# Kernel tuning notes

Hardware: AMD Instinct MI355X
Metric: run time of the kernel (lower is better)

Reference implementation:

```python
import jax, jax.numpy as jnp
import numpy as np
from jax import lax

B, T, L, H, K, NL, NB = 32, 512, 2048, 512, 3, 2, 256
PAD = (K - 1) // 2
EPS = 1e-5


def _predictor_params(key):
    k1, k2 = jax.random.split(key)
    s = 1.0 / np.sqrt(H * K).astype(np.float32)
    return dict(
        conv_w=jax.random.normal(k1, (NL, H, H, K), jnp.float32) * s,
        conv_b=jnp.zeros((NL, H), jnp.float32),
        ln_g=jnp.ones((NL, H), jnp.float32),
        ln_b=jnp.zeros((NL, H), jnp.float32),
        lin_w=jax.random.normal(k2, (H, 1), jnp.float32) * 0.02,
        lin_b=jnp.zeros((1,), jnp.float32),
    )


def setup_inputs():
    key = jax.random.key(0)
    ks = jax.random.split(key, 8)
    inp = {
        'x': jax.random.normal(ks[0], (B, T, H), jnp.float32),
        'src_mask': jnp.zeros((B, T), bool),
        'duration_target': jax.random.randint(ks[1], (B, T), 0, 8, jnp.int32),
        'pitch_target': jax.random.normal(ks[2], (B, T), jnp.float32),
        'energy_target': jax.random.uniform(ks[3], (B, T), jnp.float32),
        'max_len': L,
    }
    for name, k in zip(('dur', 'pit', 'en'), ks[4:7]):
        for p, v in _predictor_params(k).items():
            inp[name + '_' + p] = v
    inp['pitch_bins'] = jnp.linspace(-3.0, 3.0, NB - 1)
    inp['energy_bins'] = jnp.linspace(0.0, 1.0, NB - 1)
    k1, k2 = jax.random.split(ks[7])
    inp['pitch_emb'] = jax.random.normal(k1, (NB, H), jnp.float32) * 0.02
    inp['energy_emb'] = jax.random.normal(k2, (NB, H), jnp.float32) * 0.02
    return inp


def _layer_norm(h, g, b):
    m = jnp.mean(h, -1, keepdims=True)
    v = jnp.var(h, -1, keepdims=True)
    return (h - m) * lax.rsqrt(v + EPS) * g + b


def _predictor(x, cw, cb, lg, lb, lw, lbias, mask):
    # stack of [Conv1d(k=3,same) -> ReLU -> LayerNorm] x NL, then Linear -> 1
    out = x
    for i in range(NL):
        h = lax.conv_general_dilated(out.transpose(0, 2, 1), cw[i], (1,), [(PAD, PAD)],
                                     dimension_numbers=('NCH', 'OIH', 'NCH'))
        h = h.transpose(0, 2, 1) + cb[i]  # [B, T, H]
        out = _layer_norm(jax.nn.relu(h), lg[i], lb[i])
    out = (out @ lw)[..., 0] + lbias[0]  # [B, T]
    return jnp.where(mask, 0.0, out)


def _length_regulate(x, duration, max_len):
    # vectorized equivalent of the per-token expand+concat+pad loop
    csum = jnp.cumsum(duration, axis=1)                     # [B, T]
    frames = jnp.arange(max_len)                            # [L]
    idx = jax.vmap(lambda c: jnp.searchsorted(c, frames, side='right'))(csum)  # [B, L]
    idx = jnp.clip(idx, 0, x.shape[1] - 1)
    out = jnp.take_along_axis(x, idx[:, :, None], axis=1)   # [B, L, H]
    mel_len = jnp.minimum(csum[:, -1], max_len)             # [B]
    out = out * (frames[None, :] < mel_len[:, None])[..., None]
    return out, mel_len


def reference(x, src_mask, duration_target, pitch_target, energy_target, max_len,
              dur_conv_w, dur_conv_b, dur_ln_g, dur_ln_b, dur_lin_w, dur_lin_b,
              pit_conv_w, pit_conv_b, pit_ln_g, pit_ln_b, pit_lin_w, pit_lin_b,
              en_conv_w, en_conv_b, en_ln_g, en_ln_b, en_lin_w, en_lin_b,
              pitch_bins, energy_bins, pitch_emb, energy_emb):
    log_d = _predictor(x, dur_conv_w, dur_conv_b, dur_ln_g, dur_ln_b, dur_lin_w, dur_lin_b, src_mask)
    pitch_pred = _predictor(x, pit_conv_w, pit_conv_b, pit_ln_g, pit_ln_b, pit_lin_w, pit_lin_b, src_mask)
    energy_pred = _predictor(x, en_conv_w, en_conv_b, en_ln_g, en_ln_b, en_lin_w, en_lin_b, src_mask)
    # torch.bucketize(target, bins) (right=False) == searchsorted side='left'
    p_emb = pitch_emb[jnp.searchsorted(pitch_bins, pitch_target, side='left')]
    e_emb = energy_emb[jnp.searchsorted(energy_bins, energy_target, side='left')]
    x2 = x + p_emb + e_emb
    out, mel_len = _length_regulate(x2, duration_target, max_len)
    return (out, pitch_pred, energy_pred, log_d, mel_len)
```

## Files before the change

kernel.cpp:

```cpp
#include <hip/hip_runtime.h>
#include <hip/hip_bf16.h>

#define B_ 32
#define T_ 512
#define TP_ 514
#define L_ 2048
#define H_ 512
#define NRR (B_*T_)
#define KC_ 1536
#define NB_ 256
#define EPS_ 1e-5f
#define XPE ((size_t)B_ * TP_ * H_)

typedef __bf16 bf16;
typedef __bf16 bf16x8 __attribute__((ext_vector_type(8)));
typedef float f32x4 __attribute__((ext_vector_type(4)));

static const size_t WC_BYTES  = (size_t)6 * H_ * KC_ * 2;
static const size_t XP_BYTES  = XPE * 2;
static const size_t Y_BYTES   = (size_t)3 * NRR * H_ * 2;

__device__ __forceinline__ void gload16(const void* g, void* l) {
    __builtin_amdgcn_global_load_lds(
        (const __attribute__((address_space(1))) unsigned int*)g,
        (__attribute__((address_space(3))) unsigned int*)l, 16, 0, 0);
}

__global__ void k_prep_wc(const float* __restrict__ wd, const float* __restrict__ wp,
                          const float* __restrict__ we, bf16* __restrict__ wc) {
    int e = blockIdx.x * 256 + threadIdx.x;
    if (e >= 6 * H_ * KC_) return;
    int m   = e / (H_ * KC_);
    int rem = e % (H_ * KC_);
    int o  = rem / KC_;
    int r2 = rem % KC_;
    int k  = r2 / H_;
    int c  = r2 % H_;
    int p = m >> 1, i = m & 1;
    const float* w = (p == 0) ? wd : (p == 1 ? wp : we);
    float v = w[((size_t)i * H_ * H_ + (size_t)o * H_ + c) * 3 + k];
    wc[e] = (bf16)v;
}

__global__ void k_pad(const float* __restrict__ x, bf16* __restrict__ xp0,
                      bf16* __restrict__ xp1) {
    int wid = threadIdx.x >> 6, lane = threadIdx.x & 63;
    int row = blockIdx.x * 4 + wid;
    int b = row / TP_, tp = row % TP_;
    bf16* d0 = xp0 + (size_t)row * H_ + lane * 8;
    if (tp == 0 || tp == TP_ - 1) {
        bf16x8 z;
#pragma unroll
        for (int i = 0; i < 8; ++i) z[i] = (bf16)0.0f;
        *(bf16x8*)d0 = z;
#pragma unroll
        for (int p = 0; p < 3; ++p)
            *(bf16x8*)(xp1 + p * XPE + (size_t)row * H_ + lane * 8) = z;
    } else {
        const f32x4* p = (const f32x4*)(x + ((size_t)(b * T_ + tp - 1)) * H_ + lane * 8);
        f32x4 u = p[0], v = p[1];
        bf16x8 o;
        o[0] = (bf16)u[0]; o[1] = (bf16)u[1]; o[2] = (bf16)u[2]; o[3] = (bf16)u[3];
        o[4] = (bf16)v[0]; o[5] = (bf16)v[1]; o[6] = (bf16)v[2]; o[7] = (bf16)v[3];
        *(bf16x8*)d0 = o;
    }
}

__global__ void k_scan(const int* __restrict__ dur, int* __restrict__ csum,
                       float* __restrict__ mel_out) {
    int b = blockIdx.x, t = threadIdx.x;
    __shared__ int s[T_];
    s[t] = dur[b * T_ + t];
    __syncthreads();
    for (int off = 1; off < T_; off <<= 1) {
        int v = (t >= off) ? s[t - off] : 0;
        __syncthreads();
        s[t] += v;
        __syncthreads();
    }
    csum[b * T_ + t] = s[t];
    if (t == T_ - 1) mel_out[b] = (float)((s[t] < L_) ? s[t] : L_);
}

__global__ void k_gather(const float* __restrict__ x, const float* __restrict__ pemb,
                         const float* __restrict__ eemb, const float* __restrict__ pt,
                         const float* __restrict__ et, const float* __restrict__ pbins,
                         const float* __restrict__ ebins, const int* __restrict__ csum,
                         float* __restrict__ out) {
    int bi = blockIdx.x;
    int b  = bi >> 9;
    int l0 = (bi & 511) << 2;
    __shared__ int cs[T_];
    __shared__ float pb[NB_ - 1], eb[NB_ - 1];
    cs[threadIdx.x]       = csum[b * T_ + threadIdx.x];
    cs[threadIdx.x + 256] = csum[b * T_ + threadIdx.x + 256];
    if (threadIdx.x < NB_ - 1) {
        pb[threadIdx.x] = pbins[threadIdx.x];
        eb[threadIdx.x] = ebins[threadIdx.x];
    }
    __syncthreads();
    int wid = threadIdx.x >> 6, lane = threadIdx.x & 63;
    int l = l0 + wid;
    int mel = cs[T_ - 1]; if (mel > L_) mel = L_;
    float* op = out + ((size_t)(b * L_ + l)) * H_ + lane * 8;
    if (l >= mel) {
        f32x4 z = {0.f, 0.f, 0.f, 0.f};
        ((f32x4*)op)[0] = z;
        ((f32x4*)op)[1] = z;
        return;
    }
    int lo = 0, hi = T_;
    while (lo < hi) { int mid = (lo + hi) >> 1; if (cs[mid] <= l) lo = mid + 1; else hi = mid; }
    int idx = (lo < T_ - 1) ? lo : (T_ - 1);
    int rr = b * T_ + idx;
    float pv = pt[rr], ev = et[rr];
    int pi, ei;
    { int a = 0, c = NB_ - 1; while (a < c) { int mid = (a + c) >> 1; if (pb[mid] < pv) a = mid + 1; else c = mid; } pi = a; }
    { int a = 0, c = NB_ - 1; while (a < c) { int mid = (a + c) >> 1; if (eb[mid] < ev) a = mid + 1; else c = mid; } ei = a; }
    const f32x4* xp = (const f32x4*)(x    + (size_t)rr * H_ + lane * 8);
    const f32x4* pp = (const f32x4*)(pemb + (size_t)pi * H_ + lane * 8);
    const f32x4* ep = (const f32x4*)(eemb + (size_t)ei * H_ + lane * 8);
    ((f32x4*)op)[0] = xp[0] + pp[0] + ep[0];
    ((f32x4*)op)[1] = xp[1] + pp[1] + ep[1];
}

template<int LAYER>
__global__ __launch_bounds__(256)
void k_gemm(const bf16* __restrict__ Xp, const bf16* __restrict__ Wall,
            const float* __restrict__ cb0, const float* __restrict__ cb1,
            const float* __restrict__ cb2, bf16* __restrict__ Y) {
    __shared__ bf16 lA[136 * 64];
    __shared__ bf16 lB[3 * 128 * 64];

    int bid = blockIdx.x;
    int xcd = bid & 7, idx = bid >> 3;
    int colblk = idx >> 4;
    int rowblk = xcd * 16 + (idx & 15);
    int p  = colblk >> 2;
    int oB = (colblk & 3) * 128;
    int rowBase = rowblk * 128;

    const bf16* A = (LAYER == 0) ? Xp : (Xp + (size_t)p * XPE);
    const bf16* W = Wall + ((size_t)(2 * p + LAYER) * H_ + oB) * KC_;
    const float* cbp  = (p == 0) ? cb0 : (p == 1 ? cb1 : cb2);
    const float* bias = cbp + LAYER * H_;

    int tid = threadIdx.x;
    int wid = tid >> 6, lane = tid & 63;
    int wm = wid >> 1, wn = wid & 1;
    int lr = lane & 15, kq = lane >> 4;
    int rsub = lane >> 3;
    int csw  = ((lane & 7) ^ rsub) << 3;
    int b = rowBase >> 9, t0 = rowBase & (T_ - 1);
    const bf16* Abase = A + ((size_t)(b * TP_ + t0)) * H_;

    f32x4 acc[4][4];
#pragma unroll
    for (int m = 0; m < 4; ++m)
#pragma unroll
        for (int n = 0; n < 4; ++n) acc[m][n] = (f32x4){0.f, 0.f, 0.f, 0.f};

    for (int s = 0; s < 8; ++s) {
        int c0 = s * 64;
#pragma unroll
        for (int q = 0; q < 5; ++q) {
            int g = q * 4 + wid;
            if (g < 17)
                gload16(Abase + (size_t)(g * 8 + rsub) * H_ + c0 + csw, &lA[g * 8 * 64]);
        }
#pragma unroll
        for (int tap = 0; tap < 3; ++tap)
#pragma unroll
            for (int q = 0; q < 4; ++q) {
                int g = q * 4 + wid;
                gload16(W + (size_t)(g * 8 + rsub) * KC_ + tap * H_ + c0 + csw,
                        &lB[(tap * 128 + g * 8) * 64]);
            }
        __syncthreads();

#pragma unroll
        for (int tap = 0; tap < 3; ++tap) {
            bf16x8 af[4][2], bfr[4][2];
            int ka = (lr + tap) & 7, kb = lr & 7;
#pragma unroll
            for (int m = 0; m < 4; ++m)
#pragma unroll
                for (int kk = 0; kk < 2; ++kk)
                    af[m][kk] = *(const bf16x8*)&lA[(wm * 64 + m * 16 + lr + tap) * 64 +
                                                    ((((kk * 4 + kq) ^ ka)) << 3)];
#pragma unroll
            for (int n = 0; n < 4; ++n)
#pragma unroll
                for (int kk = 0; kk < 2; ++kk)
                    bfr[n][kk] = *(const bf16x8*)&lB[(tap * 128 + wn * 64 + n * 16 + lr) * 64 +
                                                     ((((kk * 4 + kq) ^ kb)) << 3)];
#pragma unroll
            for (int m = 0; m < 4; ++m)
#pragma unroll
                for (int n = 0; n < 4; ++n)
#pragma unroll
                    for (int kk = 0; kk < 2; ++kk)
                        acc[m][n] = __builtin_amdgcn_mfma_f32_16x16x32_bf16(
                            af[m][kk], bfr[n][kk], acc[m][n], 0, 0, 0);
        }
        __syncthreads();
    }

#pragma unroll
    for (int n = 0; n < 4; ++n) {
        int o = oB + wn * 64 + n * 16 + lr;
        float bi = bias[o];
#pragma unroll
        for (int m = 0; m < 4; ++m) {
            int row = rowBase + wm * 64 + m * 16 + 4 * kq;
#pragma unroll
            for (int r = 0; r < 4; ++r)
                Y[((size_t)p * NRR + row + r) * H_ + o] = (bf16)fmaxf(acc[m][n][r] + bi, 0.f);
        }
    }
}

__global__ void k_ln_store(const bf16* __restrict__ Yin,
                           const float* __restrict__ g0, const float* __restrict__ g1,
                           const float* __restrict__ g2,
                           const float* __restrict__ bb0, const float* __restrict__ bb1,
                           const float* __restrict__ bb2, bf16* __restrict__ xp1) {
    int wid = threadIdx.x >> 6, lane = threadIdx.x & 63;
    int rg = blockIdx.x * 4 + wid;
    int p = rg >> 14, r = rg & (NRR - 1);
    const float* g   = (p == 0) ? g0 : (p == 1 ? g1 : g2);
    const float* bta = (p == 0) ? bb0 : (p == 1 ? bb1 : bb2);
    bf16x8 a = *(const bf16x8*)(Yin + ((size_t)p * NRR + r) * H_ + lane * 8);
    float f[8];
#pragma unroll
    for (int i = 0; i < 8; ++i) f[i] = (float)a[i];
    float s1 = 0.f, s2 = 0.f;
#pragma unroll
    for (int i = 0; i < 8; ++i) { s1 += f[i]; s2 += f[i] * f[i]; }
    for (int m = 1; m < 64; m <<= 1) { s1 += __shfl_xor(s1, m); s2 += __shfl_xor(s2, m); }
    float mean = s1 * (1.f / H_);
    float var  = s2 * (1.f / H_) - mean * mean;
    float rs   = rsqrtf(var + EPS_);
    const f32x4* gp = (const f32x4*)g;
    const f32x4* bp = (const f32x4*)bta;
    f32x4 ga = gp[lane * 2], gb = gp[lane * 2 + 1];
    f32x4 ba = bp[lane * 2], bbv = bp[lane * 2 + 1];
    bf16x8 o;
    o[0] = (bf16)((f[0] - mean) * rs * ga[0] + ba[0]);
    o[1] = (bf16)((f[1] - mean) * rs * ga[1] + ba[1]);
    o[2] = (bf16)((f[2] - mean) * rs * ga[2] + ba[2]);
    o[3] = (bf16)((f[3] - mean) * rs * ga[3] + ba[3]);
    o[4] = (bf16)((f[4] - mean) * rs * gb[0] + bbv[0]);
    o[5] = (bf16)((f[5] - mean) * rs * gb[1] + bbv[1]);
    o[6] = (bf16)((f[6] - mean) * rs * gb[2] + bbv[2]);
    o[7] = (bf16)((f[7] - mean) * rs * gb[3] + bbv[3]);
    int bb = r >> 9, t = r & (T_ - 1);
    *(bf16x8*)(xp1 + (size_t)p * XPE + ((size_t)(bb * TP_ + t + 1)) * H_ + lane * 8) = o;
}

__global__ void k_ln_linear(const bf16* __restrict__ Yin,
                            const float* __restrict__ g0, const float* __restrict__ g1,
                            const float* __restrict__ g2,
                            const float* __restrict__ bb0, const float* __restrict__ bb1,
                            const float* __restrict__ bb2,
                            const float* __restrict__ w0p, const float* __restrict__ w1p,
                            const float* __restrict__ w2p,
                            const float* __restrict__ lb0, const float* __restrict__ lb1,
                            const float* __restrict__ lb2,
                            const unsigned char* __restrict__ mask,
                            float* __restrict__ o0, float* __restrict__ o1,
                            float* __restrict__ o2) {
    int wid = threadIdx.x >> 6, lane = threadIdx.x & 63;
    int rg = blockIdx.x * 4 + wid;
    int p = rg >> 14, r = rg & (NRR - 1);
    const float* g   = ((p == 0) ? g0 : (p == 1 ? g1 : g2)) + H_;
    const float* bta = ((p == 0) ? bb0 : (p == 1 ? bb1 : bb2)) + H_;
    const float* lw  = (p == 0) ? w0p : (p == 1 ? w1p : w2p);
    const float* lb  = (p == 0) ? lb0 : (p == 1 ? lb1 : lb2);
    float*       op  = (p == 0) ? o0 : (p == 1 ? o1 : o2);
    bf16x8 a = *(const bf16x8*)(Yin + ((size_t)p * NRR + r) * H_ + lane * 8);
    float f[8];
#pragma unroll
    for (int i = 0; i < 8; ++i) f[i] = (float)a[i];
    float s1 = 0.f, s2 = 0.f;
#pragma unroll
    for (int i = 0; i < 8; ++i) { s1 += f[i]; s2 += f[i] * f[i]; }
    for (int m = 1; m < 64; m <<= 1) { s1 += __shfl_xor(s1, m); s2 += __shfl_xor(s2, m); }
    float mean = s1 * (1.f / H_);
    float var  = s2 * (1.f / H_) - mean * mean;
    float rs   = rsqrtf(var + EPS_);
    const f32x4* gp = (const f32x4*)g;
    const f32x4* bp = (const f32x4*)bta;
    const f32x4* wp = (const f32x4*)lw;
    f32x4 ga = gp[lane * 2], gb = gp[lane * 2 + 1];
    f32x4 ba = bp[lane * 2], bbv = bp[lane * 2 + 1];
    f32x4 wa = wp[lane * 2], wb = wp[lane * 2 + 1];
    float s = ((f[0] - mean) * rs * ga[0] + ba[0]) * wa[0]
            + ((f[1] - mean) * rs * ga[1] + ba[1]) * wa[1]
            + ((f[2] - mean) * rs * ga[2] + ba[2]) * wa[2]
            + ((f[3] - mean) * rs * ga[3] + ba[3]) * wa[3]
            + ((f[4] - mean) * rs * gb[0] + bbv[0]) * wb[0]
            + ((f[5] - mean) * rs * gb[1] + bbv[1]) * wb[1]
            + ((f[6] - mean) * rs * gb[2] + bbv[2]) * wb[2]
            + ((f[7] - mean) * rs * gb[3] + bbv[3]) * wb[3];
    for (int m = 1; m < 64; m <<= 1) s += __shfl_xor(s, m);
    if (lane == 0) op[r] = mask[r] ? 0.f : (s + lb[0]);
}

extern "C" void kernel_launch(void* const* d_in, const int* in_sizes, int n_in,
                              void* d_out, int out_size, void* d_ws, size_t ws_size,
                              hipStream_t stream) {
    const float* x  = (const float*)d_in[0];
    const unsigned char* mask = (const unsigned char*)d_in[1];
    const int*   dur = (const int*)d_in[2];
    const float* pt  = (const float*)d_in[3];
    const float* et  = (const float*)d_in[4];
    const float* cw[3]    = {(const float*)d_in[6],  (const float*)d_in[12], (const float*)d_in[18]};
    const float* cb[3]    = {(const float*)d_in[7],  (const float*)d_in[13], (const float*)d_in[19]};
    const float* lg[3]    = {(const float*)d_in[8],  (const float*)d_in[14], (const float*)d_in[20]};
    const float* lbn[3]   = {(const float*)d_in[9],  (const float*)d_in[15], (const float*)d_in[21]};
    const float* lw[3]    = {(const float*)d_in[10], (const float*)d_in[16], (const float*)d_in[22]};
    const float* lbias[3] = {(const float*)d_in[11], (const float*)d_in[17], (const float*)d_in[23]};
    const float* pbins = (const float*)d_in[24];
    const float* ebins = (const float*)d_in[25];
    const float* pemb  = (const float*)d_in[26];
    const float* eemb  = (const float*)d_in[27];

    float* out0 = (float*)d_out;
    const size_t OUT0 = (size_t)B_ * L_ * H_;
    float* pitch_out  = out0 + OUT0;
    float* energy_out = pitch_out + NRR;
    float* logd_out   = energy_out + NRR;
    float* mel_out    = logd_out + NRR;

    char* ws = (char*)d_ws;
    bf16*  wc   = (bf16*)ws;
    bf16*  xp0  = (bf16*)(ws + WC_BYTES);
    bf16*  xp1  = (bf16*)(ws + WC_BYTES + XP_BYTES);
    bf16*  y    = (bf16*)(ws + WC_BYTES + 4 * XP_BYTES);
    int*   csum = (int*)(ws + WC_BYTES + 4 * XP_BYTES + Y_BYTES);

    k_prep_wc<<<(6 * H_ * KC_ + 255) / 256, 256, 0, stream>>>(cw[0], cw[1], cw[2], wc);
    k_pad<<<B_ * TP_ / 4, 256, 0, stream>>>(x, xp0, xp1);
    k_scan<<<B_, T_, 0, stream>>>(dur, csum, mel_out);
    k_gather<<<B_ * L_ / 4, 256, 0, stream>>>(x, pemb, eemb, pt, et, pbins, ebins, csum, out0);

    k_gemm<0><<<1536, 256, 0, stream>>>(xp0, wc, cb[0], cb[1], cb[2], y);
    k_ln_store<<<3 * NRR / 4, 256, 0, stream>>>(y, lg[0], lg[1], lg[2],
                                                lbn[0], lbn[1], lbn[2], xp1);
    k_gemm<1><<<1536, 256, 0, stream>>>(xp1, wc, cb[0], cb[1], cb[2], y);
    k_ln_linear<<<3 * NRR / 4, 256, 0, stream>>>(y, lg[0], lg[1], lg[2],
                                                 lbn[0], lbn[1], lbn[2],
                                                 lw[0], lw[1], lw[2],
                                                 lbias[0], lbias[1], lbias[2],
                                                 mask, logd_out, pitch_out, energy_out);
}
```

Baseline: 246.1 us.

## Prepack conv weights in MFMA fragment order and load B directly from global

Weights are repacked during prep into per-column-block sections laid out in the exact per-lane MFMA B-fragment order. The GEMM drops its LDS staging buffer for B and has each lane read its bf16x8 fragments straight from global memory. This cuts LDS traffic and footprint, which could allow more resident blocks. The cost is that every wave now issues its own global/L2 loads for B with no sharing through LDS, and those loads sit on the MFMA critical path.

```diff
diff --git a/kernel.cpp b/kernel.cpp
--- a/kernel.cpp
+++ b/kernel.cpp
@@ -11,6 +11,7 @@
 #define NB_ 256
 #define EPS_ 1e-5f
 #define XPE ((size_t)B_ * TP_ * H_)
+#define WSEC 196608
 
 typedef __bf16 bf16;
 typedef __bf16 bf16x8 __attribute__((ext_vector_type(8)));
@@ -30,16 +31,20 @@
                           const float* __restrict__ we, bf16* __restrict__ wc) {
     int e = blockIdx.x * 256 + threadIdx.x;
     if (e >= 6 * H_ * KC_) return;
-    int m   = e / (H_ * KC_);
-    int rem = e % (H_ * KC_);
-    int o  = rem / KC_;
-    int r2 = rem % KC_;
-    int k  = r2 / H_;
-    int c  = r2 % H_;
+    int sec = e / WSEC, r = e % WSEC;
+    int m = sec >> 2, colblk = sec & 3;
+    int j  = r & 7;
+    int l  = (r >> 3) & 63;
+    int n  = (r >> 9) & 3;
+    int wn = (r >> 11) & 1;
+    int kk = (r >> 12) & 1;
+    int t13 = r >> 13;
+    int tap = t13 % 3, hc = t13 / 3;
+    int o = colblk * 128 + wn * 64 + n * 16 + (l & 15);
+    int c = hc * 64 + kk * 32 + (l >> 4) * 8 + j;
     int p = m >> 1, i = m & 1;
     const float* w = (p == 0) ? wd : (p == 1 ? wp : we);
-    float v = w[((size_t)i * H_ * H_ + (size_t)o * H_ + c) * 3 + k];
-    wc[e] = (bf16)v;
+    wc[e] = (bf16)w[((size_t)(i * H_ + o) * H_ + c) * 3 + tap];
 }
 
 __global__ void k_pad(const float* __restrict__ x, bf16* __restrict__ xp0,
@@ -130,7 +135,6 @@
             const float* __restrict__ cb0, const float* __restrict__ cb1,
             const float* __restrict__ cb2, bf16* __restrict__ Y) {
     __shared__ bf16 lA[136 * 64];
-    __shared__ bf16 lB[3 * 128 * 64];
 
     int bid = blockIdx.x;
     int xcd = bid & 7, idx = bid >> 3;
@@ -141,7 +145,7 @@
     int rowBase = rowblk * 128;
 
     const bf16* A = (LAYER == 0) ? Xp : (Xp + (size_t)p * XPE);
-    const bf16* W = Wall + ((size_t)(2 * p + LAYER) * H_ + oB) * KC_;
+    const bf16* Wsec = Wall + (size_t)((2 * p + LAYER) * 4 + (colblk & 3)) * WSEC;
     const float* cbp  = (p == 0) ? cb0 : (p == 1 ? cb1 : cb2);
     const float* bias = cbp + LAYER * H_;
 
@@ -153,6 +157,7 @@
     int csw  = ((lane & 7) ^ rsub) << 3;
     int b = rowBase >> 9, t0 = rowBase & (T_ - 1);
     const bf16* Abase = A + ((size_t)(b * TP_ + t0)) * H_;
+    const bf16* Wlane = Wsec + (size_t)wn * 2048 + lane * 8;
 
     f32x4 acc[4][4];
 #pragma unroll
@@ -168,32 +173,25 @@
             if (g < 17)
                 gload16(Abase + (size_t)(g * 8 + rsub) * H_ + c0 + csw, &lA[g * 8 * 64]);
         }
-#pragma unroll
-        for (int tap = 0; tap < 3; ++tap)
-#pragma unroll
-            for (int q = 0; q < 4; ++q) {
-                int g = q * 4 + wid;
-                gload16(W + (size_t)(g * 8 + rsub) * KC_ + tap * H_ + c0 + csw,
-                        &lB[(tap * 128 + g * 8) * 64]);
-            }
+        const bf16* Wh = Wlane + (size_t)s * 24576;
         __syncthreads();
 
 #pragma unroll
         for (int tap = 0; tap < 3; ++tap) {
             bf16x8 af[4][2], bfr[4][2];
-            int ka = (lr + tap) & 7, kb = lr & 7;
+            int ka = (lr + tap) & 7;
+#pragma unroll
+            for (int n = 0; n < 4; ++n)
+#pragma unroll
+                for (int kk = 0; kk < 2; ++kk)
+                    bfr[n][kk] = *(const bf16x8*)&Wh[((size_t)(tap * 2 + kk) * 2) * 2048 +
+                                                     n * 512];
 #pragma unroll
             for (int m = 0; m < 4; ++m)
 #pragma unroll
                 for (int kk = 0; kk < 2; ++kk)
                     af[m][kk] = *(const bf16x8*)&lA[(wm * 64 + m * 16 + lr + tap) * 64 +
                                                     ((((kk * 4 + kq) ^ ka)) << 3)];
-#pragma unroll
-            for (int n = 0; n < 4; ++n)
-#pragma unroll
-                for (int kk = 0; kk < 2; ++kk)
-                    bfr[n][kk] = *(const bf16x8*)&lB[(tap * 128 + wn * 64 + n * 16 + lr) * 64 +
-                                                     ((((kk * 4 + kq) ^ kb)) << 3)];
 #pragma unroll
             for (int m = 0; m < 4; ++m)
 #pragma unroll
```

After: 265.2 us. 1.08x slower.

## Fuse layer-2 LayerNorm+Linear reduction into GEMM epilogue via per-row partial sums

Applied to the files above, without the earlier changes.

The second conv GEMM no longer writes its bf16 activations. Its epilogue instead computes per-row partial sums (sum, sum of squares, and a gamma*w-weighted sum) over each 128-column tile and stores them to a small buffer. A tiny finalize kernel then combines the four column-tile partials and applies the LayerNorm+Linear algebraically, folding gamma*w and beta*w into constants. This removes the layer-2 Y write and reread and one full-size kernel, at the cost of extra shuffles and a shared-memory reduction in the epilogue, and variance computed as E[x^2]-mean^2 in fp32.

```diff
diff --git a/kernel.cpp b/kernel.cpp
--- a/kernel.cpp
+++ b/kernel.cpp
@@ -128,7 +128,12 @@
 __global__ __launch_bounds__(256)
 void k_gemm(const bf16* __restrict__ Xp, const bf16* __restrict__ Wall,
             const float* __restrict__ cb0, const float* __restrict__ cb1,
-            const float* __restrict__ cb2, bf16* __restrict__ Y) {
+            const float* __restrict__ cb2,
+            const float* __restrict__ g0, const float* __restrict__ g1,
+            const float* __restrict__ g2,
+            const float* __restrict__ w0p, const float* __restrict__ w1p,
+            const float* __restrict__ w2p,
+            bf16* __restrict__ Y, float* __restrict__ part) {
     __shared__ bf16 lA[136 * 64];
     __shared__ bf16 lB[3 * 128 * 64];
 
@@ -206,16 +211,59 @@
         __syncthreads();
     }
 
-#pragma unroll
-    for (int n = 0; n < 4; ++n) {
-        int o = oB + wn * 64 + n * 16 + lr;
-        float bi = bias[o];
-#pragma unroll
-        for (int m = 0; m < 4; ++m) {
-            int row = rowBase + wm * 64 + m * 16 + 4 * kq;
-#pragma unroll
-            for (int r = 0; r < 4; ++r)
-                Y[((size_t)p * NRR + row + r) * H_ + o] = (bf16)fmaxf(acc[m][n][r] + bi, 0.f);
+    if constexpr (LAYER == 0) {
+#pragma unroll
+        for (int n = 0; n < 4; ++n) {
+            int o = oB + wn * 64 + n * 16 + lr;
+            float bi = bias[o];
+#pragma unroll
+            for (int m = 0; m < 4; ++m) {
+                int row = rowBase + wm * 64 + m * 16 + 4 * kq;
+#pragma unroll
+                for (int r = 0; r < 4; ++r)
+                    Y[((size_t)p * NRR + row + r) * H_ + o] = (bf16)fmaxf(acc[m][n][r] + bi, 0.f);
+            }
+        }
+    } else {
+        const float* gp  = ((p == 0) ? g0 : (p == 1 ? g1 : g2)) + H_;
+        const float* lwp = (p == 0) ? w0p : (p == 1 ? w1p : w2p);
+        float bc[4], gc[4], wc4[4];
+#pragma unroll
+        for (int n = 0; n < 4; ++n) {
+            int col = oB + wn * 64 + n * 16 + lr;
+            bc[n] = bias[col]; gc[n] = gp[col]; wc4[n] = lwp[col];
+        }
+        float* red = (float*)lA;
+#pragma unroll
+        for (int m = 0; m < 4; ++m)
+#pragma unroll
+            for (int r = 0; r < 4; ++r) {
+                float s = 0.f, q = 0.f, pw = 0.f;
+#pragma unroll
+                for (int n = 0; n < 4; ++n) {
+                    float v = fmaxf(acc[m][n][r] + bc[n], 0.f);
+                    s += v; q += v * v; pw += v * gc[n] * wc4[n];
+                }
+#pragma unroll
+                for (int msk = 1; msk < 16; msk <<= 1) {
+                    s  += __shfl_xor(s,  msk);
+                    q  += __shfl_xor(q,  msk);
+                    pw += __shfl_xor(pw, msk);
+                }
+                if (lr == 0) {
+                    int rl = wm * 64 + m * 16 + 4 * kq + r;
+                    red[(rl * 2 + wn) * 3 + 0] = s;
+                    red[(rl * 2 + wn) * 3 + 1] = q;
+                    red[(rl * 2 + wn) * 3 + 2] = pw;
+                }
+            }
+        __syncthreads();
+        if (tid < 128) {
+            float S = red[tid * 6 + 0] + red[tid * 6 + 3];
+            float Q = red[tid * 6 + 1] + red[tid * 6 + 4];
+            float P = red[tid * 6 + 2] + red[tid * 6 + 5];
+            float* dst = part + ((size_t)(p * NRR + rowBase + tid) * 4 + (colblk & 3)) * 3;
+            dst[0] = S; dst[1] = Q; dst[2] = P;
         }
     }
 }
@@ -258,53 +306,47 @@
     *(bf16x8*)(xp1 + (size_t)p * XPE + ((size_t)(bb * TP_ + t + 1)) * H_ + lane * 8) = o;
 }
 
-__global__ void k_ln_linear(const bf16* __restrict__ Yin,
-                            const float* __restrict__ g0, const float* __restrict__ g1,
-                            const float* __restrict__ g2,
-                            const float* __restrict__ bb0, const float* __restrict__ bb1,
-                            const float* __restrict__ bb2,
-                            const float* __restrict__ w0p, const float* __restrict__ w1p,
-                            const float* __restrict__ w2p,
-                            const float* __restrict__ lb0, const float* __restrict__ lb1,
-                            const float* __restrict__ lb2,
-                            const unsigned char* __restrict__ mask,
-                            float* __restrict__ o0, float* __restrict__ o1,
-                            float* __restrict__ o2) {
-    int wid = threadIdx.x >> 6, lane = threadIdx.x & 63;
-    int rg = blockIdx.x * 4 + wid;
-    int p = rg >> 14, r = rg & (NRR - 1);
-    const float* g   = ((p == 0) ? g0 : (p == 1 ? g1 : g2)) + H_;
-    const float* bta = ((p == 0) ? bb0 : (p == 1 ? bb1 : bb2)) + H_;
-    const float* lw  = (p == 0) ? w0p : (p == 1 ? w1p : w2p);
-    const float* lb  = (p == 0) ? lb0 : (p == 1 ? lb1 : lb2);
-    float*       op  = (p == 0) ? o0 : (p == 1 ? o1 : o2);
-    bf16x8 a = *(const bf16x8*)(Yin + ((size_t)p * NRR + r) * H_ + lane * 8);
-    float f[8];
-#pragma unroll
-    for (int i = 0; i < 8; ++i) f[i] = (float)a[i];
-    float s1 = 0.f, s2 = 0.f;
-#pragma unroll
-    for (int i = 0; i < 8; ++i) { s1 += f[i]; s2 += f[i] * f[i]; }
-    for (int m = 1; m < 64; m <<= 1) { s1 += __shfl_xor(s1, m); s2 += __shfl_xor(s2, m); }
-    float mean = s1 * (1.f / H_);
-    float var  = s2 * (1.f / H_) - mean * mean;
+__global__ void k_fin(const float* __restrict__ part,
+                      const float* __restrict__ g0, const float* __restrict__ g1,
+                      const float* __restrict__ g2,
+                      const float* __restrict__ bb0, const float* __restrict__ bb1,
+                      const float* __restrict__ bb2,
+                      const float* __restrict__ w0p, const float* __restrict__ w1p,
+                      const float* __restrict__ w2p,
+                      const float* __restrict__ lb0, const float* __restrict__ lb1,
+                      const float* __restrict__ lb2,
+                      const unsigned char* __restrict__ mask,
+                      float* __restrict__ o0, float* __restrict__ o1,
+                      float* __restrict__ o2) {
+    int blk = blockIdx.x;
+    int p = blk >> 6;
+    int r0 = (blk & 63) * 256;
+    const float* g  = ((p == 0) ? g0 : (p == 1 ? g1 : g2)) + H_;
+    const float* bt = ((p == 0) ? bb0 : (p == 1 ? bb1 : bb2)) + H_;
+    const float* w  = (p == 0) ? w0p : (p == 1 ? w1p : w2p);
+    const float* lb = (p == 0) ? lb0 : (p == 1 ? lb1 : lb2);
+    float* op       = (p == 0) ? o0 : (p == 1 ? o1 : o2);
+
+    __shared__ float sG[4], sB[4];
+    int tid = threadIdx.x, lane = tid & 63, wid = tid >> 6;
+    float gs = g[tid] * w[tid] + g[tid + 256] * w[tid + 256];
+    float bs = bt[tid] * w[tid] + bt[tid + 256] * w[tid + 256];
+    for (int m = 1; m < 64; m <<= 1) { gs += __shfl_xor(gs, m); bs += __shfl_xor(bs, m); }
+    if (lane == 0) { sG[wid] = gs; sB[wid] = bs; }
+    __syncthreads();
+    float G  = sG[0] + sG[1] + sG[2] + sG[3];
+    float Bc = sB[0] + sB[1] + sB[2] + sB[3];
+
+    int r = r0 + tid;
+    const float* pr = part + ((size_t)(p * NRR + r) * 4) * 3;
+    float S = pr[0] + pr[3] + pr[6] + pr[9];
+    float Q = pr[1] + pr[4] + pr[7] + pr[10];
+    float P = pr[2] + pr[5] + pr[8] + pr[11];
+    float mean = S * (1.f / H_);
+    float var  = Q * (1.f / H_) - mean * mean;
     float rs   = rsqrtf(var + EPS_);
-    const f32x4* gp = (const f32x4*)g;
-    const f32x4* bp = (const f32x4*)bta;
-    const f32x4* wp = (const f32x4*)lw;
-    f32x4 ga = gp[lane * 2], gb = gp[lane * 2 + 1];
-    f32x4 ba = bp[lane * 2], bbv = bp[lane * 2 + 1];
-    f32x4 wa = wp[lane * 2], wb = wp[lane * 2 + 1];
-    float s = ((f[0] - mean) * rs * ga[0] + ba[0]) * wa[0]
-            + ((f[1] - mean) * rs * ga[1] + ba[1]) * wa[1]
-            + ((f[2] - mean) * rs * ga[2] + ba[2]) * wa[2]
-            + ((f[3] - mean) * rs * ga[3] + ba[3]) * wa[3]
-            + ((f[4] - mean) * rs * gb[0] + bbv[0]) * wb[0]
-            + ((f[5] - mean) * rs * gb[1] + bbv[1]) * wb[1]
-            + ((f[6] - mean) * rs * gb[2] + bbv[2]) * wb[2]
-            + ((f[7] - mean) * rs * gb[3] + bbv[3]) * wb[3];
-    for (int m = 1; m < 64; m <<= 1) s += __shfl_xor(s, m);
-    if (lane == 0) op[r] = mask[r] ? 0.f : (s + lb[0]);
+    float val  = rs * (P - mean * G) + Bc + lb[0];
+    op[r] = mask[r] ? 0.f : val;
 }
 
 extern "C" void kernel_launch(void* const* d_in, const int* in_sizes, int n_in,
@@ -339,19 +381,24 @@
     bf16*  xp1  = (bf16*)(ws + WC_BYTES + XP_BYTES);
     bf16*  y    = (bf16*)(ws + WC_BYTES + 4 * XP_BYTES);
     int*   csum = (int*)(ws + WC_BYTES + 4 * XP_BYTES + Y_BYTES);
+    float* part = (float*)(csum + NRR);
 
     k_prep_wc<<<(6 * H_ * KC_ + 255) / 256, 256, 0, stream>>>(cw[0], cw[1], cw[2], wc);
     k_pad<<<B_ * TP_ / 4, 256, 0, stream>>>(x, xp0, xp1);
     k_scan<<<B_, T_, 0, stream>>>(dur, csum, mel_out);
     k_gather<<<B_ * L_ / 4, 256, 0, stream>>>(x, pemb, eemb, pt, et, pbins, ebins, csum, out0);
 
-    k_gemm<0><<<1536, 256, 0, stream>>>(xp0, wc, cb[0], cb[1], cb[2], y);
+    k_gemm<0><<<1536, 256, 0, stream>>>(xp0, wc, cb[0], cb[1], cb[2],
+                                        lg[0], lg[1], lg[2], lw[0], lw[1], lw[2],
+                                        y, part);
     k_ln_store<<<3 * NRR / 4, 256, 0, stream>>>(y, lg[0], lg[1], lg[2],
                                                 lbn[0], lbn[1], lbn[2], xp1);
-    k_gemm<1><<<1536, 256, 0, stream>>>(xp1, wc, cb[0], cb[1], cb[2], y);
-    k_ln_linear<<<3 * NRR / 4, 256, 0, stream>>>(y, lg[0], lg[1], lg[2],
-                                                 lbn[0], lbn[1], lbn[2],
-                                                 lw[0], lw[1], lw[2],
-                                                 lbias[0], lbias[1], lbias[2],
-                                                 mask, logd_out, pitch_out, energy_out);
-}
+    k_gemm<1><<<1536, 256, 0, stream>>>(xp1, wc, cb[0], cb[1], cb[2],
+                                        lg[0], lg[1], lg[2], lw[0], lw[1], lw[2],
+                                        y, part);
+    k_fin<<<192, 256, 0, stream>>>(part, lg[0], lg[1], lg[2],
+                                   lbn[0], lbn[1], lbn[2],
+                                   lw[0], lw[1], lw[2],
+                                   lbias[0], lbias[1], lbias[2],
+                                   mask, logd_out, pitch_out, energy_out);
+}
```

New measurement: 245.4 us. About the same (-0.3%).
